# Performance work log

Hardware: AMD Instinct MI355X
Metric: run time of the kernel (lower is better)

## Reference

```python
import jax, jax.numpy as jnp
import numpy as np

NUM_CONTEXT = 8  # context panels; +1 choice -> 9 panels, 72 ordered pairs (i != j)

_PAIRS = np.array([(i, j) for i in range(9) for j in range(9) if i != j], dtype=np.int32)
I_IDX = jnp.asarray(_PAIRS[:, 0])  # [72]
J_IDX = jnp.asarray(_PAIRS[:, 1])  # [72]


def setup_inputs() -> dict:
    key = jax.random.key(0)
    ks = jax.random.split(key, 10)
    B, C, F, H = 256, 8, 512, 256
    s_in = 1.0 / np.sqrt(2 * F)
    s_h = 1.0 / np.sqrt(H)
    return {
        "context_features": jax.random.normal(ks[0], (B, NUM_CONTEXT, F), jnp.float32),
        "choice_features": jax.random.normal(ks[1], (B, C, F), jnp.float32),
        "W1": jax.random.uniform(ks[2], (2 * F, H), jnp.float32, -s_in, s_in),
        "b1": jax.random.uniform(ks[3], (H,), jnp.float32, -s_in, s_in),
        "W2": jax.random.uniform(ks[4], (H, H), jnp.float32, -s_h, s_h),
        "b2": jax.random.uniform(ks[5], (H,), jnp.float32, -s_h, s_h),
        "W3": jax.random.uniform(ks[6], (H, H), jnp.float32, -s_h, s_h),
        "b3": jax.random.uniform(ks[7], (H,), jnp.float32, -s_h, s_h),
        "W4": jax.random.uniform(ks[8], (H, 1), jnp.float32, -s_h, s_h),
        "b4": jax.random.uniform(ks[9], (1,), jnp.float32, -s_h, s_h),
    }


def reference(context_features, choice_features, W1, b1, W2, b2, W3, b3, W4, b4):
    B, C, F = choice_features.shape[0], choice_features.shape[1], choice_features.shape[2]
    # panels[b, c, p, f]: 8 context panels + 1 choice panel per candidate choice
    ctx = jnp.broadcast_to(context_features[:, None, :, :], (B, C, NUM_CONTEXT, F))
    panels = jnp.concatenate([ctx, choice_features[:, :, None, :]], axis=2)  # [B,C,9,F]
    # all 72 ordered pairs (i != j), concatenated features -> [B,C,72,2F]
    pair = jnp.concatenate([panels[:, :, I_IDX, :], panels[:, :, J_IDX, :]], axis=-1)
    # g_theta MLP
    h = jax.nn.relu(pair @ W1 + b1)
    h = jax.nn.relu(h @ W2 + b2)        # [B,C,72,H]
    agg = h.mean(axis=2)                # [B,C,H]
    # f_phi MLP (dropout is identity in eval mode)
    g = jax.nn.relu(agg @ W3 + b3)
    score = g @ W4 + b4                 # [B,C,1]
    return score[..., 0]                # [B,C]
```

## Files before the change

kernel.cpp:

```cpp
#include <hip/hip_runtime.h>
#include <hip/hip_bf16.h>


typedef __bf16 bf16_t;
typedef bf16_t bf16x8 __attribute__((ext_vector_type(8)));
typedef bf16_t bf16x4 __attribute__((ext_vector_type(4)));
typedef float f32x4 __attribute__((ext_vector_type(4)));

#define MFMA16(a, b, c) __builtin_amdgcn_mfma_f32_16x16x32_bf16((a), (b), (c), 0, 0, 0)

__global__ __launch_bounds__(256) void prep_kernel(
    const float* __restrict__ ctx, const float* __restrict__ cho,
    const float* __restrict__ W1, const float* __restrict__ W2,
    const float* __restrict__ W3, bf16_t* __restrict__ Xb,
    bf16_t* __restrict__ Wp, bf16_t* __restrict__ W2T,
    bf16_t* __restrict__ W3T) {
  const int blk = blockIdx.x;
  const int t = threadIdx.x;
  if (blk < 2048) {
    const int row = blk * 2 + (t >> 7);
    const int c4 = (t & 127) * 4;
    const int bi = row >> 4;
    const int p = row & 15;
    const float* src = (p < 8) ? ctx + (size_t)(bi * 8 + p) * 512 + c4
                               : cho + (size_t)(bi * 8 + (p - 8)) * 512 + c4;
    const f32x4 x = *(const f32x4*)src;
    bf16x4 y;
    for (int e = 0; e < 4; ++e) y[e] = (bf16_t)x[e];
    *(bf16x4*)(Xb + (size_t)row * 512 + c4) = y;
  } else {
    const int idx = (blk - 2048) * 256 + t;
    if (idx < 262144) {
      const int j = idx >> 9, k = idx & 511;
      const float v = (j < 256) ? W1[k * 256 + j] : W1[(512 + k) * 256 + (j - 256)];
      Wp[idx] = (bf16_t)v;
    } else if (idx < 327680) {
      const int s = idx - 262144;
      const int n = s >> 8, k = s & 255;
      W2T[s] = (bf16_t)W2[k * 256 + n];
    } else {
      const int s = idx - 327680;
      const int n = s >> 8, k = s & 255;
      W3T[s] = (bf16_t)W3[k * 256 + n];
    }
  }
}

__global__ __launch_bounds__(256) void k1_kernel(
    const bf16_t* __restrict__ Xb, const bf16_t* __restrict__ Wp,
    float* __restrict__ UV) {
  const int bm = blockIdx.x & 63;
  const int bn = blockIdx.x >> 6;
  const int t = threadIdx.x;
  const int lane = t & 63;
  const int w = t >> 6;
  const int col = lane & 15;
  const int quad = lane >> 4;
  f32x4 acc[4][2] = {};
  for (int ks = 0; ks < 16; ++ks) {
    const int k = ks * 32 + quad * 8;
    bf16x8 af[4], bf[2];
    for (int mt = 0; mt < 4; ++mt) {
      const int r = bm * 64 + mt * 16 + col;
      af[mt] = *(const bf16x8*)(Xb + (size_t)r * 512 + k);
    }
    for (int nt = 0; nt < 2; ++nt) {
      const int n = bn * 128 + (w * 2 + nt) * 16 + col;
      bf[nt] = *(const bf16x8*)(Wp + (size_t)n * 512 + k);
    }
    for (int mt = 0; mt < 4; ++mt)
      for (int nt = 0; nt < 2; ++nt)
        acc[mt][nt] = MFMA16(af[mt], bf[nt], acc[mt][nt]);
  }
  for (int mt = 0; mt < 4; ++mt)
    for (int nt = 0; nt < 2; ++nt) {
      const int n = bn * 128 + (w * 2 + nt) * 16 + col;
      for (int reg = 0; reg < 4; ++reg) {
        const int r = bm * 64 + mt * 16 + quad * 4 + reg;
        UV[(size_t)r * 512 + n] = acc[mt][nt][reg];
      }
    }
}

__global__ __launch_bounds__(512) void k2_kernel(
    const float* __restrict__ UV, const float* __restrict__ b1,
    const float* __restrict__ b2, const bf16_t* __restrict__ W2T,
    bf16_t* __restrict__ aggb) {
  __shared__ bf16_t h1[192][136];
  __shared__ float S[9][256];
  const int b = blockIdx.x;
  const int t = threadIdx.x;
  const int lane = t & 63;
  const int w = t >> 6;
  const int col = lane & 15;
  const int quad = lane >> 4;
  const float* su = nullptr;
  const float* sv = nullptr;
  int sr = 0, sc0 = 0;
  if (t < 384) {
    sr = t >> 1;
    sc0 = (t & 1) * 64;
    if (sr < 56) {
      const int i = sr / 7;
      const int jj = sr - i * 7;
      const int j = jj + (jj >= i ? 1 : 0);
      su = UV + (size_t)(b * 16 + i) * 512;
      sv = UV + (size_t)(b * 16 + j) * 512 + 256;
    } else if (sr >= 64) {
      const int ch = (sr - 64) >> 4;
      const int rr = (sr - 64) & 15;
      if (rr < 8) {
        su = UV + (size_t)(b * 16 + 8 + ch) * 512;
        sv = UV + (size_t)(b * 16 + rr) * 512 + 256;
      } else {
        su = UV + (size_t)(b * 16 + (rr - 8)) * 512;
        sv = UV + (size_t)(b * 16 + 8 + ch) * 512 + 256;
      }
    }
  }
  const int mtb = (w & 1) * 6;
  const int q = w >> 1;
  f32x4 acc[6][4] = {};
  for (int half = 0; half < 2; ++half) {
    const int kbase = half * 128;
    if (t < 384) {
      if (su) {
        for (int c = sc0; c < sc0 + 64; c += 4) {
          const f32x4 uu = *(const f32x4*)(su + kbase + c);
          const f32x4 vv = *(const f32x4*)(sv + kbase + c);
          const f32x4 bb = *(const f32x4*)(b1 + kbase + c);
          bf16x4 y;
          for (int e = 0; e < 4; ++e) y[e] = (bf16_t)fmaxf(uu[e] + vv[e] + bb[e], 0.0f);
          *(bf16x4*)(&h1[sr][c]) = y;
        }
      } else {
        for (int c = sc0; c < sc0 + 64; c += 4)
          *(bf16x4*)(&h1[sr][c]) = (bf16x4)0.0f;
      }
    }
    __syncthreads();
    for (int ks = 0; ks < 4; ++ks) {
      const int k = ks * 32 + quad * 8;
      bf16x8 af[6], bf[4];
      for (int mt = 0; mt < 6; ++mt)
        af[mt] = *(const bf16x8*)(&h1[(mtb + mt) * 16 + col][k]);
      for (int nt = 0; nt < 4; ++nt) {
        const int n = q * 64 + nt * 16 + col;
        bf[nt] = *(const bf16x8*)(W2T + (size_t)n * 256 + kbase + k);
      }
      for (int mt = 0; mt < 6; ++mt)
        for (int nt = 0; nt < 4; ++nt)
          acc[mt][nt] = MFMA16(af[mt], bf[nt], acc[mt][nt]);
    }
    __syncthreads();
  }
  for (int nt = 0; nt < 4; ++nt) {
    const int n = q * 64 + nt * 16 + col;
    const float b2c = b2[n];
    float sctx = 0.0f;
    for (int mt = 0; mt < 6; ++mt) {
      const int gm = mtb + mt;
      float s = 0.0f;
      for (int reg = 0; reg < 4; ++reg) {
        const int row = gm * 16 + quad * 4 + reg;
        if (row < 56 || row >= 64) s += fmaxf(acc[mt][nt][reg] + b2c, 0.0f);
      }
      s += __shfl_xor(s, 16);
      s += __shfl_xor(s, 32);
      if (gm < 4) {
        sctx += s;
      } else if (lane < 16) {
        S[1 + (gm - 4)][n] = s;
      }
    }
    if (mtb == 0 && lane < 16) S[0][n] = sctx;
  }
  __syncthreads();
  {
    const int ch = t >> 6;
    const int n0 = (t & 63) * 4;
    bf16x4 y;
    for (int e = 0; e < 4; ++e)
      y[e] = (bf16_t)((S[0][n0 + e] + S[1 + ch][n0 + e]) * (1.0f / 72.0f));
    *(bf16x4*)(aggb + (size_t)(b * 8 + ch) * 256 + n0) = y;
  }
}

__global__ __launch_bounds__(256) void k3_kernel(
    const bf16_t* __restrict__ aggb, const bf16_t* __restrict__ W3T,
    const float* __restrict__ b3, const float* __restrict__ W4,
    const float* __restrict__ b4, float* __restrict__ out) {
  __shared__ float red[4][64];
  const int blk = blockIdx.x;
  const int t = threadIdx.x;
  const int lane = t & 63;
  const int w = t >> 6;
  const int col = lane & 15;
  const int quad = lane >> 4;
  f32x4 acc[4][4] = {};
  for (int ks = 0; ks < 8; ++ks) {
    const int k = ks * 32 + quad * 8;
    bf16x8 af[4], bf[4];
    for (int mt = 0; mt < 4; ++mt)
      af[mt] = *(const bf16x8*)(aggb + (size_t)(blk * 64 + mt * 16 + col) * 256 + k);
    for (int nt = 0; nt < 4; ++nt) {
      const int n = (w * 4 + nt) * 16 + col;
      bf[nt] = *(const bf16x8*)(W3T + (size_t)n * 256 + k);
    }
    for (int mt = 0; mt < 4; ++mt)
      for (int nt = 0; nt < 4; ++nt)
        acc[mt][nt] = MFMA16(af[mt], bf[nt], acc[mt][nt]);
  }
  float pr[4][4];
  for (int mt = 0; mt < 4; ++mt)
    for (int reg = 0; reg < 4; ++reg) pr[mt][reg] = 0.0f;
  for (int nt = 0; nt < 4; ++nt) {
    const int n = (w * 4 + nt) * 16 + col;
    const float b3c = b3[n];
    const float w4c = W4[n];
    for (int mt = 0; mt < 4; ++mt)
      for (int reg = 0; reg < 4; ++reg)
        pr[mt][reg] += fmaxf(acc[mt][nt][reg] + b3c, 0.0f) * w4c;
  }
  for (int mt = 0; mt < 4; ++mt)
    for (int reg = 0; reg < 4; ++reg) {
      float s = pr[mt][reg];
      s += __shfl_xor(s, 1);
      s += __shfl_xor(s, 2);
      s += __shfl_xor(s, 4);
      s += __shfl_xor(s, 8);
      if (col == 0) red[w][mt * 16 + quad * 4 + reg] = s;
    }
  __syncthreads();
  if (t < 64) out[blk * 64 + t] = red[0][t] + red[1][t] + red[2][t] + red[3][t] + b4[0];
}

extern "C" void kernel_launch(void* const* d_in, const int* in_sizes, int n_in,
                              void* d_out, int out_size, void* d_ws, size_t ws_size,
                              hipStream_t stream) {
  (void)in_sizes; (void)n_in; (void)out_size; (void)ws_size;
  const float* ctx = (const float*)d_in[0];
  const float* cho = (const float*)d_in[1];
  const float* W1  = (const float*)d_in[2];
  const float* b1  = (const float*)d_in[3];
  const float* W2  = (const float*)d_in[4];
  const float* b2  = (const float*)d_in[5];
  const float* W3  = (const float*)d_in[6];
  const float* b3  = (const float*)d_in[7];
  const float* W4  = (const float*)d_in[8];
  const float* b4  = (const float*)d_in[9];
  char* ws = (char*)d_ws;
  bf16_t* Wp   = (bf16_t*)(ws + 0);
  bf16_t* W2T  = (bf16_t*)(ws + 524288);
  bf16_t* W3T  = (bf16_t*)(ws + 655360);
  bf16_t* Xb   = (bf16_t*)(ws + 786432);
  float*  UV   = (float*)(ws + 4980736);
  bf16_t* aggb = (bf16_t*)(ws + 13369344);
  float*  out  = (float*)d_out;

  prep_kernel<<<dim3(3584), dim3(256), 0, stream>>>(ctx, cho, W1, W2, W3, Xb, Wp, W2T, W3T);
  k1_kernel<<<dim3(256), dim3(256), 0, stream>>>(Xb, Wp, UV);
  k2_kernel<<<dim3(256), dim3(512), 0, stream>>>(UV, b1, b2, W2T, aggb);
  k3_kernel<<<dim3(32), dim3(256), 0, stream>>>(aggb, W3T, b3, W4, b4, out);
}
```

Baseline: 130.4 us.

## Fuse f_phi MLP into k2 and halve k1 N-tile for more blocks

Folds the final f_phi layers (W3 GEMM, bias, ReLU, W4 dot) into the per-batch k2 kernel, so aggregated features stay in shared memory and are never written to global memory. This removes one kernel launch and the aggb round trip. Separately, k1 now gives each block a 64-column slice instead of 128, doubling its grid to 512 blocks for better CU occupancy, at the cost of reloading the A tile twice as often. The fused tail pads the MFMA M dimension from 8 rows to 16, so half of that compute is wasted, and it reuses the h1 shared-memory region.

Measured after the change: 129.5 us. Within noise of the previous version (-0.7%).

```diff
diff --git a/kernel.cpp b/kernel.cpp
--- a/kernel.cpp
+++ b/kernel.cpp
@@ -56,38 +56,36 @@
   const int w = t >> 6;
   const int col = lane & 15;
   const int quad = lane >> 4;
-  f32x4 acc[4][2] = {};
+  const int n = bn * 64 + w * 16 + col;
+  f32x4 acc[4] = {};
   for (int ks = 0; ks < 16; ++ks) {
     const int k = ks * 32 + quad * 8;
-    bf16x8 af[4], bf[2];
+    bf16x8 af[4];
     for (int mt = 0; mt < 4; ++mt) {
       const int r = bm * 64 + mt * 16 + col;
       af[mt] = *(const bf16x8*)(Xb + (size_t)r * 512 + k);
     }
-    for (int nt = 0; nt < 2; ++nt) {
-      const int n = bn * 128 + (w * 2 + nt) * 16 + col;
-      bf[nt] = *(const bf16x8*)(Wp + (size_t)n * 512 + k);
-    }
-    for (int mt = 0; mt < 4; ++mt)
-      for (int nt = 0; nt < 2; ++nt)
-        acc[mt][nt] = MFMA16(af[mt], bf[nt], acc[mt][nt]);
+    const bf16x8 bf = *(const bf16x8*)(Wp + (size_t)n * 512 + k);
+    for (int mt = 0; mt < 4; ++mt) acc[mt] = MFMA16(af[mt], bf, acc[mt]);
   }
   for (int mt = 0; mt < 4; ++mt)
-    for (int nt = 0; nt < 2; ++nt) {
-      const int n = bn * 128 + (w * 2 + nt) * 16 + col;
-      for (int reg = 0; reg < 4; ++reg) {
-        const int r = bm * 64 + mt * 16 + quad * 4 + reg;
-        UV[(size_t)r * 512 + n] = acc[mt][nt][reg];
-      }
+    for (int reg = 0; reg < 4; ++reg) {
+      const int r = bm * 64 + mt * 16 + quad * 4 + reg;
+      UV[(size_t)r * 512 + n] = acc[mt][reg];
     }
 }
 
 __global__ __launch_bounds__(512) void k2_kernel(
     const float* __restrict__ UV, const float* __restrict__ b1,
     const float* __restrict__ b2, const bf16_t* __restrict__ W2T,
-    bf16_t* __restrict__ aggb) {
-  __shared__ bf16_t h1[192][136];
-  __shared__ float S[9][256];
+    const bf16_t* __restrict__ W3T, const float* __restrict__ b3,
+    const float* __restrict__ W4, const float* __restrict__ b4,
+    float* __restrict__ out) {
+  __shared__ char smem[52224];
+  bf16_t (*h1)[136] = (bf16_t(*)[136])smem;
+  float (*S)[256] = (float(*)[256])smem;
+  bf16_t (*Ag)[264] = (bf16_t(*)[264])(smem + 9216);
+  float (*red)[8] = (float(*)[8])(smem + 9216 + 8448);
   const int b = blockIdx.x;
   const int t = threadIdx.x;
   const int lane = t & 63;
@@ -182,57 +180,38 @@
     bf16x4 y;
     for (int e = 0; e < 4; ++e)
       y[e] = (bf16_t)((S[0][n0 + e] + S[1 + ch][n0 + e]) * (1.0f / 72.0f));
-    *(bf16x4*)(aggb + (size_t)(b * 8 + ch) * 256 + n0) = y;
-  }
-}
-
-__global__ __launch_bounds__(256) void k3_kernel(
-    const bf16_t* __restrict__ aggb, const bf16_t* __restrict__ W3T,
-    const float* __restrict__ b3, const float* __restrict__ W4,
-    const float* __restrict__ b4, float* __restrict__ out) {
-  __shared__ float red[4][64];
-  const int blk = blockIdx.x;
-  const int t = threadIdx.x;
-  const int lane = t & 63;
-  const int w = t >> 6;
-  const int col = lane & 15;
-  const int quad = lane >> 4;
-  f32x4 acc[4][4] = {};
+    *(bf16x4*)(&Ag[ch][n0]) = y;
+    *(bf16x4*)(&Ag[8 + ch][n0]) = (bf16x4)0.0f;
+  }
+  __syncthreads();
+  f32x4 acc2[2] = {};
   for (int ks = 0; ks < 8; ++ks) {
     const int k = ks * 32 + quad * 8;
-    bf16x8 af[4], bf[4];
-    for (int mt = 0; mt < 4; ++mt)
-      af[mt] = *(const bf16x8*)(aggb + (size_t)(blk * 64 + mt * 16 + col) * 256 + k);
-    for (int nt = 0; nt < 4; ++nt) {
-      const int n = (w * 4 + nt) * 16 + col;
-      bf[nt] = *(const bf16x8*)(W3T + (size_t)n * 256 + k);
-    }
-    for (int mt = 0; mt < 4; ++mt)
-      for (int nt = 0; nt < 4; ++nt)
-        acc[mt][nt] = MFMA16(af[mt], bf[nt], acc[mt][nt]);
-  }
-  float pr[4][4];
-  for (int mt = 0; mt < 4; ++mt)
-    for (int reg = 0; reg < 4; ++reg) pr[mt][reg] = 0.0f;
-  for (int nt = 0; nt < 4; ++nt) {
-    const int n = (w * 4 + nt) * 16 + col;
-    const float b3c = b3[n];
-    const float w4c = W4[n];
-    for (int mt = 0; mt < 4; ++mt)
-      for (int reg = 0; reg < 4; ++reg)
-        pr[mt][reg] += fmaxf(acc[mt][nt][reg] + b3c, 0.0f) * w4c;
-  }
-  for (int mt = 0; mt < 4; ++mt)
-    for (int reg = 0; reg < 4; ++reg) {
-      float s = pr[mt][reg];
-      s += __shfl_xor(s, 1);
-      s += __shfl_xor(s, 2);
-      s += __shfl_xor(s, 4);
-      s += __shfl_xor(s, 8);
-      if (col == 0) red[w][mt * 16 + quad * 4 + reg] = s;
-    }
+    const bf16x8 af = *(const bf16x8*)(&Ag[col][k]);
+    for (int nt = 0; nt < 2; ++nt) {
+      const int n = w * 32 + nt * 16 + col;
+      const bf16x8 bf = *(const bf16x8*)(W3T + (size_t)n * 256 + k);
+      acc2[nt] = MFMA16(af, bf, acc2[nt]);
+    }
+  }
+  for (int reg = 0; reg < 4; ++reg) {
+    float pr = 0.0f;
+    for (int nt = 0; nt < 2; ++nt) {
+      const int n = w * 32 + nt * 16 + col;
+      pr += fmaxf(acc2[nt][reg] + b3[n], 0.0f) * W4[n];
+    }
+    pr += __shfl_xor(pr, 1);
+    pr += __shfl_xor(pr, 2);
+    pr += __shfl_xor(pr, 4);
+    pr += __shfl_xor(pr, 8);
+    if (col == 0 && quad < 2) red[w][quad * 4 + reg] = pr;
+  }
   __syncthreads();
-  if (t < 64) out[blk * 64 + t] = red[0][t] + red[1][t] + red[2][t] + red[3][t] + b4[0];
+  if (t < 8) {
+    float sc = b4[0];
+    for (int ww = 0; ww < 8; ++ww) sc += red[ww][t];
+    out[b * 8 + t] = sc;
+  }
 }
 
 extern "C" void kernel_launch(void* const* d_in, const int* in_sizes, int n_in,
@@ -255,11 +234,9 @@
   bf16_t* W3T  = (bf16_t*)(ws + 655360);
   bf16_t* Xb   = (bf16_t*)(ws + 786432);
   float*  UV   = (float*)(ws + 4980736);
-  bf16_t* aggb = (bf16_t*)(ws + 13369344);
   float*  out  = (float*)d_out;
 
   prep_kernel<<<dim3(3584), dim3(256), 0, stream>>>(ctx, cho, W1, W2, W3, Xb, Wp, W2T, W3T);
-  k1_kernel<<<dim3(256), dim3(256), 0, stream>>>(Xb, Wp, UV);
-  k2_kernel<<<dim3(256), dim3(512), 0, stream>>>(UV, b1, b2, W2T, aggb);
-  k3_kernel<<<dim3(32), dim3(256), 0, stream>>>(aggb, W3T, b3, W4, b4, out);
-}
+  k1_kernel<<<dim3(512), dim3(256), 0, stream>>>(Xb, Wp, UV);
+  k2_kernel<<<dim3(256), dim3(512), 0, stream>>>(UV, b1, b2, W2T, W3T, b3, W4, b4, out);
+}
```
